# Kernel tuning notes

Hardware: AMD Instinct MI355X
Metric: run time of the kernel (lower is better)

Reference implementation:

```python
import jax, jax.numpy as jnp
import numpy as np

N = 4096          # nodes == num_rels (forced by einsum 'ij,ijk->ik')
IN_F = 128
OUT_F = 128


def setup_inputs() -> dict:
    key = jax.random.key(0)
    k1, k2, k3, k4 = jax.random.split(key, 4)
    xavier = float(np.sqrt(2.0 / (IN_F + OUT_F)))
    return {
        "input": jax.random.normal(k1, (N, IN_F), dtype=jnp.float32),
        "adjacency_matrix": jax.random.uniform(k2, (N, N), dtype=jnp.float32),
        "rel_matrix": jax.random.normal(k3, (N, OUT_F, OUT_F), dtype=jnp.float32) * xavier,
        "weights": jax.random.normal(k4, (N, IN_F, OUT_F), dtype=jnp.float32) * xavier,
        "bias": jnp.zeros((OUT_F,), dtype=jnp.float32),
    }


def reference(input, adjacency_matrix, rel_matrix, weights, bias):
    # per-node transform: support[n, k] = sum_j input[n, j] * weights[n, j, k]
    support = jnp.einsum('nj,njk->nk', input, weights)          # [N, out]
    # per-node relational combine: out[n, j] = sum_k rel_matrix[n, j, k] * support[n, k]
    out = jnp.einsum('njk,nk->nj', rel_matrix, support)         # [N, out]
    # dense adjacency aggregation + bias
    out = jnp.matmul(adjacency_matrix, out) + bias              # [N, out]
    return out
```

## Files before the change

kernel.cpp:

```cpp
#include <hip/hip_runtime.h>
#include <hip/hip_bf16.h>

typedef __attribute__((ext_vector_type(4))) float floatx4;
typedef __bf16 bf16x8 __attribute__((ext_vector_type(8)));

static __device__ __forceinline__ unsigned short f2bf(float x) {
    union { float f; unsigned int u; } v; v.f = x;
    unsigned int u = v.u;
    unsigned int r = u + 0x7FFF + ((u >> 16) & 1);
    return (unsigned short)(r >> 16);
}

__global__ __launch_bounds__(256) void node_transform(
    const float* __restrict__ input,
    const float* __restrict__ rel,
    const float* __restrict__ wts,
    unsigned int* __restrict__ h_t)
{
    __shared__ float s_in[2][128];
    __shared__ float s_part[2][4][128];
    __shared__ float s_sup[2][128];
    __shared__ float s_h[2][128];

    const int tid = threadIdx.x;
    const int b = blockIdx.x;

    if (tid < 64) {
        float4 v = ((const float4*)input)[b * 64 + tid];
        ((float4*)&s_in[0][0])[tid] = v;
    }
    __syncthreads();

    const int node = tid >> 7;
    const int tl   = tid & 127;
    const int n    = b * 2 + node;

    {
        const int jg = tl >> 5;
        const int kq = tl & 31;
        const float4* W4 = (const float4*)(wts + (size_t)n * 16384);
        float4 acc = {0.f, 0.f, 0.f, 0.f};
        const int j0 = jg * 32;
        #pragma unroll 16
        for (int jj = 0; jj < 32; ++jj) {
            const int j = j0 + jj;
            const float x = s_in[node][j];
            const float4 w = W4[j * 32 + kq];
            acc.x += x * w.x; acc.y += x * w.y;
            acc.z += x * w.z; acc.w += x * w.w;
        }
        ((float4*)&s_part[node][jg][0])[kq] = acc;
    }
    __syncthreads();
    s_sup[node][tl] = s_part[node][0][tl] + s_part[node][1][tl]
                    + s_part[node][2][tl] + s_part[node][3][tl];
    __syncthreads();

    {
        const int jl = tl >> 2;
        const int kg = tl & 3;
        const float4* R4 = (const float4*)(rel + (size_t)n * 16384);
        const float4* S4 = (const float4*)&s_sup[node][0];
        #pragma unroll 2
        for (int p = 0; p < 4; ++p) {
            const int j = p * 32 + jl;
            const float4* rr = R4 + j * 32 + kg * 8;
            float acc = 0.f;
            #pragma unroll
            for (int i = 0; i < 8; ++i) {
                const float4 r = rr[i];
                const float4 s = S4[kg * 8 + i];
                acc += r.x * s.x + r.y * s.y + r.z * s.z + r.w * s.w;
            }
            acc += __shfl_xor(acc, 1);
            acc += __shfl_xor(acc, 2);
            if (kg == 0) s_h[node][j] = acc;
        }
    }
    __syncthreads();

    if (tid < 128) {
        const unsigned int lo = f2bf(s_h[0][tid]);
        const unsigned int hi = f2bf(s_h[1][tid]);
        h_t[tid * 2048 + b] = lo | (hi << 16);
    }
}

__global__ __launch_bounds__(512) void agg_gemm_splitk(
    const float* __restrict__ A,
    const unsigned short* __restrict__ ht,
    float* __restrict__ part)
{
    __shared__ __align__(16) unsigned short As[16][136];
    __shared__ __align__(16) unsigned short Bs[128][136];

    const int tid  = threadIdx.x;
    const int wave = tid >> 6;
    const int lane = tid & 63;
    const int s    = blockIdx.x & 3;
    const int m0   = (blockIdx.x >> 2) * 16;
    const int kbase = s * 1024;

    floatx4 acc = {0.f, 0.f, 0.f, 0.f};

    const int ar = tid >> 5;
    const int ac = (tid & 31) * 4;
    const int bj = tid >> 2;
    const int bs = tid & 3;

    for (int kb = kbase; kb < kbase + 1024; kb += 128) {
        __syncthreads();
        {
            const float4 v = *(const float4*)(A + (size_t)(m0 + ar) * 4096 + kb + ac);
            const unsigned int p0 = (unsigned int)f2bf(v.x) | ((unsigned int)f2bf(v.y) << 16);
            const unsigned int p1 = (unsigned int)f2bf(v.z) | ((unsigned int)f2bf(v.w) << 16);
            *(uint2*)&As[ar][ac] = make_uint2(p0, p1);
        }
        {
            const unsigned short* src = ht + (size_t)bj * 4096 + kb + bs * 8;
            #pragma unroll
            for (int i = 0; i < 4; ++i) {
                const uint4 v = *(const uint4*)(src + i * 32);
                *(uint4*)&Bs[bj][bs * 8 + i * 32] = v;
            }
        }
        __syncthreads();
        const int mn = lane & 15;
        const int kq = lane >> 4;
        const unsigned short* arow = &As[mn][kq * 8];
        const unsigned short* brow = &Bs[wave * 16 + mn][kq * 8];
        #pragma unroll
        for (int k0 = 0; k0 < 128; k0 += 32) {
            const bf16x8 af  = *(const bf16x8*)(arow + k0);
            const bf16x8 bfr = *(const bf16x8*)(brow + k0);
            acc = __builtin_amdgcn_mfma_f32_16x16x32_bf16(af, bfr, acc, 0, 0, 0);
        }
    }

    const int col = wave * 16 + (lane & 15);
    const int r0  = (lane >> 4) * 4;
    float* dst = part + ((size_t)s * 4096 + m0 + r0) * 128 + col;
    #pragma unroll
    for (int r = 0; r < 4; ++r) {
        dst[(size_t)r * 128] = acc[r];
    }
}

__global__ __launch_bounds__(256) void reduce_bias(
    const float* __restrict__ part,
    const float* __restrict__ bias,
    float* __restrict__ out)
{
    const int f = blockIdx.x * 256 + threadIdx.x;
    const float4* p4 = (const float4*)part;
    const float4 b = ((const float4*)bias)[f & 31];
    float4 s0 = p4[f];
    float4 s1 = p4[131072 + f];
    float4 s2 = p4[262144 + f];
    float4 s3 = p4[393216 + f];
    float4 r;
    r.x = s0.x + s1.x + s2.x + s3.x + b.x;
    r.y = s0.y + s1.y + s2.y + s3.y + b.y;
    r.z = s0.z + s1.z + s2.z + s3.z + b.z;
    r.w = s0.w + s1.w + s2.w + s3.w + b.w;
    ((float4*)out)[f] = r;
}

extern "C" void kernel_launch(void* const* d_in, const int* in_sizes, int n_in,
                              void* d_out, int out_size, void* d_ws, size_t ws_size,
                              hipStream_t stream) {
    const float* input = (const float*)d_in[0];
    const float* adj   = (const float*)d_in[1];
    const float* rel   = (const float*)d_in[2];
    const float* wts   = (const float*)d_in[3];
    const float* bias  = (const float*)d_in[4];
    float* out = (float*)d_out;

    unsigned int* h_t = (unsigned int*)d_ws;
    float* part = (float*)((char*)d_ws + (1 << 20));

    node_transform<<<2048, 256, 0, stream>>>(input, rel, wts, h_t);
    agg_gemm_splitk<<<1024, 512, 0, stream>>>(adj, (const unsigned short*)d_ws, part);
    reduce_bias<<<512, 256, 0, stream>>>(part, bias, out);
}
```

Baseline: 593.0 us.

## Process one node per block with fully coalesced weight and relation reads

The node transform kernel now uses one block per node instead of two. Each thread reads consecutive float4 elements of the weight and relation matrices (tid-indexed stride), so each wavefront load is a single contiguous segment. Partial results are reduced through a padded shared-memory buffer, and each block writes one 16-bit value per output feature instead of a packed pair. The aim is better streaming bandwidth on the 512 MB of weight and relation data, at the cost of twice as many blocks, more shared-memory reduction work and uncoalesced 2-byte scattered stores.

```diff
diff --git a/kernel.cpp b/kernel.cpp
--- a/kernel.cpp
+++ b/kernel.cpp
@@ -15,74 +15,61 @@
     const float* __restrict__ input,
     const float* __restrict__ rel,
     const float* __restrict__ wts,
-    unsigned int* __restrict__ h_t)
+    unsigned short* __restrict__ h_t)
 {
-    __shared__ float s_in[2][128];
-    __shared__ float s_part[2][4][128];
-    __shared__ float s_sup[2][128];
-    __shared__ float s_h[2][128];
+    __shared__ float s_in[128];
+    __shared__ float s_sup[128];
+    __shared__ __align__(16) float s_big[4224];
 
     const int tid = threadIdx.x;
-    const int b = blockIdx.x;
+    const int n   = blockIdx.x;
+    const int l   = tid & 31;
+    const int g   = tid >> 5;
 
-    if (tid < 64) {
-        float4 v = ((const float4*)input)[b * 64 + tid];
-        ((float4*)&s_in[0][0])[tid] = v;
+    if (tid < 32) {
+        ((float4*)s_in)[tid] = ((const float4*)(input + (size_t)n * 128))[tid];
     }
     __syncthreads();
 
-    const int node = tid >> 7;
-    const int tl   = tid & 127;
-    const int n    = b * 2 + node;
-
     {
-        const int jg = tl >> 5;
-        const int kq = tl & 31;
         const float4* W4 = (const float4*)(wts + (size_t)n * 16384);
         float4 acc = {0.f, 0.f, 0.f, 0.f};
-        const int j0 = jg * 32;
-        #pragma unroll 16
-        for (int jj = 0; jj < 32; ++jj) {
-            const int j = j0 + jj;
-            const float x = s_in[node][j];
-            const float4 w = W4[j * 32 + kq];
+        #pragma unroll 8
+        for (int i = 0; i < 16; ++i) {
+            const int j = i * 8 + g;
+            const float  x = s_in[j];
+            const float4 w = W4[i * 256 + tid];
             acc.x += x * w.x; acc.y += x * w.y;
             acc.z += x * w.z; acc.w += x * w.w;
         }
-        ((float4*)&s_part[node][jg][0])[kq] = acc;
+        ((float4*)&s_big[g * 128])[l] = acc;
     }
     __syncthreads();
-    s_sup[node][tl] = s_part[node][0][tl] + s_part[node][1][tl]
-                    + s_part[node][2][tl] + s_part[node][3][tl];
+    if (tid < 128) {
+        float s = 0.f;
+        #pragma unroll
+        for (int g2 = 0; g2 < 8; ++g2) s += s_big[g2 * 128 + tid];
+        s_sup[tid] = s;
+    }
     __syncthreads();
 
     {
-        const int jl = tl >> 2;
-        const int kg = tl & 3;
         const float4* R4 = (const float4*)(rel + (size_t)n * 16384);
-        const float4* S4 = (const float4*)&s_sup[node][0];
-        #pragma unroll 2
-        for (int p = 0; p < 4; ++p) {
-            const int j = p * 32 + jl;
-            const float4* rr = R4 + j * 32 + kg * 8;
-            float acc = 0.f;
-            #pragma unroll
-            for (int i = 0; i < 8; ++i) {
-                const float4 r = rr[i];
-                const float4 s = S4[kg * 8 + i];
-                acc += r.x * s.x + r.y * s.y + r.z * s.z + r.w * s.w;
-            }
-            acc += __shfl_xor(acc, 1);
-            acc += __shfl_xor(acc, 2);
-            if (kg == 0) s_h[node][j] = acc;
+        const float4  sv = ((const float4*)s_sup)[l];
+        #pragma unroll 8
+        for (int i = 0; i < 16; ++i) {
+            const int j = i * 8 + g;
+            const float4 r = R4[i * 256 + tid];
+            const float p = r.x * sv.x + r.y * sv.y + r.z * sv.z + r.w * sv.w;
+            s_big[j * 33 + l] = p;
         }
     }
     __syncthreads();
-
     if (tid < 128) {
-        const unsigned int lo = f2bf(s_h[0][tid]);
-        const unsigned int hi = f2bf(s_h[1][tid]);
-        h_t[tid * 2048 + b] = lo | (hi << 16);
+        float h = 0.f;
+        #pragma unroll
+        for (int m = 0; m < 32; ++m) h += s_big[tid * 33 + m];
+        h_t[(size_t)tid * 4096 + n] = f2bf(h);
     }
 }
 
@@ -176,10 +163,10 @@
     const float* bias  = (const float*)d_in[4];
     float* out = (float*)d_out;
 
-    unsigned int* h_t = (unsigned int*)d_ws;
+    unsigned short* h_t = (unsigned short*)d_ws;
     float* part = (float*)((char*)d_ws + (1 << 20));
 
-    node_transform<<<2048, 256, 0, stream>>>(input, rel, wts, h_t);
+    node_transform<<<4096, 256, 0, stream>>>(input, rel, wts, h_t);
     agg_gemm_splitk<<<1024, 512, 0, stream>>>(adj, (const unsigned short*)d_ws, part);
     reduce_bias<<<512, 256, 0, stream>>>(part, bias, out);
 }
```

Result: faster. 570.0 us (-3.9%).
